# Performance work log

Hardware: AMD Instinct MI355X
Metric: run time of the kernel (lower is better)

The kernel has to match this reference:

```python
import jax, jax.numpy as jnp
import numpy as np

EMB = 1024
H = 16
D = EMB // H  # 64
EPS = 1e-5
SM_SCALE = 1.0  # forward default sm_scale=1.0
CAUSAL = True
NEG = -1e30


def _layernorm(t, g, b):
    # LayerNorm over last dim (head_dim), per torch nn.LayerNorm(head_dim)
    m = jnp.mean(t, axis=-1, keepdims=True)
    v = jnp.mean(jnp.square(t - m), axis=-1, keepdims=True)
    return (t - m) * jax.lax.rsqrt(v + EPS) * g + b


def setup_inputs() -> dict:
    key = jax.random.key(0)
    ks = jax.random.split(key, 8)
    N, L = 2, 2048
    x = jax.random.normal(ks[0], (N, L, EMB), dtype=jnp.float32)
    mask = jnp.ones((N, L), dtype=jnp.int32)  # accepted but unused, as in the torch module
    s = 0.02
    Wq = jax.random.normal(ks[1], (EMB, EMB), dtype=jnp.float32) * s
    Wk = jax.random.normal(ks[2], (EMB, EMB), dtype=jnp.float32) * s
    Wv = jax.random.normal(ks[3], (EMB, EMB), dtype=jnp.float32) * s
    Wo = jax.random.normal(ks[4], (EMB, EMB), dtype=jnp.float32) * s
    bo = jnp.zeros((EMB,), dtype=jnp.float32)
    gq = jnp.ones((D,), dtype=jnp.float32)
    bq = jnp.zeros((D,), dtype=jnp.float32)
    gk = jnp.ones((D,), dtype=jnp.float32)
    bk = jnp.zeros((D,), dtype=jnp.float32)
    return {"x": x, "mask": mask, "Wq": Wq, "Wk": Wk, "Wv": Wv,
            "gq": gq, "bq": bq, "gk": gk, "bk": bk, "Wo": Wo, "bo": bo}


def reference(x, mask, Wq, Wk, Wv, gq, bq, gk, bk, Wo, bo):
    N, L, _ = x.shape
    # QKV projections (torch Linear: x @ W.T), split into heads -> [N, H, L, D]
    q = (x @ Wq.T).reshape(N, L, H, D).transpose(0, 2, 1, 3)
    k = (x @ Wk.T).reshape(N, L, H, D).transpose(0, 2, 1, 3)
    v = (x @ Wv.T).reshape(N, L, H, D).transpose(0, 2, 1, 3)
    # fused_q_norm variant: per-head LayerNorm on Q and K (fused into attention kernel)
    q = _layernorm(q, gq, bq)
    k = _layernorm(k, gk, bk)
    scores = jnp.einsum('nhld,nhmd->nhlm', q, k) * SM_SCALE  # [N,H,L,L]
    if CAUSAL:
        causal = jnp.tril(jnp.ones((L, L), dtype=bool))
        scores = jnp.where(causal, scores, NEG)
    attn = jax.nn.softmax(scores, axis=-1)
    out = jnp.einsum('nhlm,nhmd->nhld', attn, v)
    out = out.transpose(0, 2, 1, 3).reshape(N, L, EMB)
    return out @ Wo.T + bo
```

## Files before the change

kernel.cpp:

```cpp
#include <hip/hip_runtime.h>
#include <stdint.h>

typedef unsigned short u16;
typedef u16   u16x4    __attribute__((ext_vector_type(4)));
typedef u16   u16x8    __attribute__((ext_vector_type(8)));
typedef u16x8 u16x8_ma __attribute__((may_alias));
typedef __bf16 bf16x8  __attribute__((ext_vector_type(8)));
typedef float f32x4    __attribute__((ext_vector_type(4)));
typedef f32x4 f32x4_ma __attribute__((may_alias));

#define EMB    1024
#define NHEAD  16
#define HD     64
#define SEQ    2048
#define NBATCH 2
#define ROWS   (NBATCH*SEQ)
#define SATT   72
#define TSTRIDE 132

__device__ __forceinline__ u16 f2b(float f) {
  uint32_t u; __builtin_memcpy(&u, &f, 4);
  u = u + 0x7fffu + ((u >> 16) & 1u);
  return (u16)(u >> 16);
}
__device__ __forceinline__ u16x8 ld8(const u16* p) { return *(const u16x8_ma*)p; }
__device__ __forceinline__ void  st8(u16* p, u16x8 v) { *(u16x8_ma*)p = v; }
__device__ __forceinline__ bf16x8 asbf(u16x8 v) {
  union { u16x8 u; bf16x8 b; } c; c.u = v; return c.b;
}
__device__ __forceinline__ uint32_t cvtpk(float a, float b) {
  uint32_t r;
  asm("v_cvt_pk_bf16_f32 %0, %1, %2" : "=v"(r) : "v"(a), "v"(b));
  return r;
}
__device__ __forceinline__ void async_cp16(const u16* g, u16* l) {
  __builtin_amdgcn_global_load_lds(
      (const __attribute__((address_space(1))) void*)g,
      (__attribute__((address_space(3))) void*)l, 16, 0, 0);
}

__global__ __launch_bounds__(256) void cvt_all(
    const float* __restrict__ x,
    const float* __restrict__ w0, const float* __restrict__ w1,
    const float* __restrict__ w2, const float* __restrict__ w3,
    u16* __restrict__ xd, u16* __restrict__ d0, u16* __restrict__ d1,
    u16* __restrict__ d2, u16* __restrict__ d3)
{
  int bid = blockIdx.x;
  const float* s; u16* d; int off;
  if (bid < 4096) { s = x; d = xd; off = bid; }
  else {
    int t = bid - 4096; int m = t >> 10; off = t & 1023;
    switch (m) {
      case 0: s = w0; d = d0; break;
      case 1: s = w1; d = d1; break;
      case 2: s = w2; d = d2; break;
      default: s = w3; d = d3; break;
    }
  }
  size_t i = ((size_t)off * 256 + threadIdx.x) * 4;
  f32x4 v = *(const f32x4_ma*)(s + i);
  u16x4 o;
  #pragma unroll
  for (int j = 0; j < 4; j++) o[j] = f2b(v[j]);
  *(u16x4*)(d + i) = o;
}

template<int AMODE>
__device__ __forceinline__ void gemm_acc_128x128(
    const u16* __restrict__ A, const u16* __restrict__ B,
    int m0, int n0, u16* As, u16* Bs, f32x4 acc[4][4])
{
  const int tid  = threadIdx.x;
  const int lane = tid & 63;
  const int wave = tid >> 6;
  const int wm   = (wave >> 1) * 64;
  const int wn   = (wave & 1) * 64;
  const int ar   = tid >> 2;
  const int ac   = (tid & 3) * 8;
  const int lm   = lane & 15;
  const int lk   = (lane >> 4) * 8;

  #pragma unroll
  for (int i = 0; i < 4; i++)
    #pragma unroll
    for (int j = 0; j < 4; j++)
      #pragma unroll
      for (int e = 0; e < 4; e++) acc[i][j][e] = 0.f;

  for (int k0 = 0; k0 < EMB; k0 += 64) {
    size_t a0[2], a1[2];
    #pragma unroll
    for (int pnl = 0; pnl < 2; pnl++) {
      int kc = k0 + pnl * 32 + ac;
      if (AMODE == 0) {
        a0[pnl] = (size_t)(m0 + ar)      * EMB + kc;
        a1[pnl] = (size_t)(m0 + ar + 64) * EMB + kc;
      } else {
        int h = kc >> 6, d = kc & 63;
        int r0 = m0 + ar, r1 = m0 + ar + 64;
        a0[pnl] = (((size_t)((r0 >> 11) * NHEAD + h)) * SEQ + (r0 & (SEQ-1))) * HD + d;
        a1[pnl] = (((size_t)((r1 >> 11) * NHEAD + h)) * SEQ + (r1 & (SEQ-1))) * HD + d;
      }
    }
    __syncthreads();
    #pragma unroll
    for (int pnl = 0; pnl < 2; pnl++) {
      const int pb = pnl * 4096;
      async_cp16(A + a0[pnl], As + pb + tid * 8);
      async_cp16(A + a1[pnl], As + pb + (tid + 256) * 8);
      async_cp16(B + (size_t)(n0 + ar)      * EMB + k0 + pnl * 32 + ac, Bs + pb + tid * 8);
      async_cp16(B + (size_t)(n0 + ar + 64) * EMB + k0 + pnl * 32 + ac, Bs + pb + (tid + 256) * 8);
    }
    __syncthreads();

    #pragma unroll
    for (int pnl = 0; pnl < 2; pnl++) {
      const int pb = pnl * 4096;
      bf16x8 af[4], bfr[4];
      #pragma unroll
      for (int i = 0; i < 4; i++)
        af[i] = asbf(ld8(As + pb + (wm + i * 16 + lm) * 32 + lk));
      #pragma unroll
      for (int j = 0; j < 4; j++)
        bfr[j] = asbf(ld8(Bs + pb + (wn + j * 16 + lm) * 32 + lk));
      #pragma unroll
      for (int i = 0; i < 4; i++)
        #pragma unroll
        for (int j = 0; j < 4; j++)
          acc[i][j] = __builtin_amdgcn_mfma_f32_16x16x32_bf16(af[i], bfr[j], acc[i][j], 0, 0, 0);
    }
  }
}

__device__ __forceinline__ void epilogue_scatter_ln(
    f32x4 acc[4][4], u16* dst, int m0, int n0, int head_base, int Hdst,
    const float* g, const float* b, int do_ln)
{
  const int lane = threadIdx.x & 63, wave = threadIdx.x >> 6;
  const int wm = (wave >> 1) * 64, wn = (wave & 1) * 64;
  const int lm = lane & 15, quad = lane >> 4;

  float gv[4], bv[4];
  #pragma unroll
  for (int j = 0; j < 4; j++) { gv[j] = g[j * 16 + lm]; bv[j] = b[j * 16 + lm]; }

  #pragma unroll
  for (int i = 0; i < 4; i++)
    #pragma unroll
    for (int r = 0; r < 4; r++) {
      float val[4];
      #pragma unroll
      for (int j = 0; j < 4; j++) val[j] = acc[i][j][r];
      if (do_ln) {
        float s = val[0] + val[1] + val[2] + val[3];
        #pragma unroll
        for (int o = 8; o >= 1; o >>= 1) s += __shfl_xor(s, o, 64);
        float mean = s * (1.f / 64.f);
        float ss = 0.f;
        #pragma unroll
        for (int j = 0; j < 4; j++) { val[j] -= mean; ss += val[j] * val[j]; }
        #pragma unroll
        for (int o = 8; o >= 1; o >>= 1) ss += __shfl_xor(ss, o, 64);
        float inv = rsqrtf(ss * (1.f / 64.f) + 1e-5f);
        #pragma unroll
        for (int j = 0; j < 4; j++) val[j] = val[j] * inv * gv[j] + bv[j];
      }
      int row = m0 + wm + i * 16 + quad * 4 + r;
      int bn = row >> 11, l = row & (SEQ - 1);
      #pragma unroll
      for (int j = 0; j < 4; j++) {
        int col = n0 + wn + j * 16 + lm;
        int hl = (col >> 6) - head_base, d = col & 63;
        dst[(((size_t)(bn * Hdst + hl)) * SEQ + l) * HD + d] = f2b(val[j]);
      }
    }
}

__device__ __forceinline__ void epilogue_transpose_v(
    f32x4 acc[4][4], u16* dst, int m0, int n0, int Hdst, u16* Ts)
{
  const int tid = threadIdx.x, lane = tid & 63, wave = tid >> 6;
  const int wm = (wave >> 1) * 64;
  const int lm = lane & 15, quad = lane >> 4;
  const int bn = m0 >> 11, l0 = m0 & (SEQ - 1);

  #pragma unroll
  for (int pass = 0; pass < 2; ++pass) {
    __syncthreads();
    if ((wave & 1) == pass) {
      #pragma unroll
      for (int i = 0; i < 4; i++)
        #pragma unroll
        for (int j = 0; j < 4; j++)
          #pragma unroll
          for (int r = 0; r < 4; r++)
            Ts[(j * 16 + lm) * TSTRIDE + wm + i * 16 + quad * 4 + r] =
                f2b(acc[i][j][r]);
    }
    __syncthreads();
    const int hl = (n0 >> 6) + pass;
    u16* base = dst + ((size_t)(bn * Hdst + hl)) * HD * SEQ + l0;
    #pragma unroll
    for (int it = 0; it < 4; ++it) {
      int e = it * 2048 + tid * 8;
      int d = e >> 7, l = e & 127;
      st8(base + (size_t)d * SEQ + l, ld8(Ts + d * TSTRIDE + l));
    }
  }
}

__global__ __launch_bounds__(256) void gemm_qkv(
    const u16* __restrict__ x,
    const u16* __restrict__ Wq, const u16* __restrict__ Wk, const u16* __restrict__ Wv,
    const float* __restrict__ gq, const float* __restrict__ bq,
    const float* __restrict__ gk, const float* __restrict__ bk,
    u16* __restrict__ qd, u16* __restrict__ kb, u16* __restrict__ vb)
{
  __shared__ __align__(16) u16 As[128 * 64];
  __shared__ __align__(16) u16 Bs[128 * 64];
  __shared__ __align__(16) u16 Ts[64 * TSTRIDE];
  const int m0 = blockIdx.y * 128, n0 = blockIdx.x * 128;
  f32x4 acc[4][4];
  if (blockIdx.z == 0) {
    gemm_acc_128x128<0>(x, Wq, m0, n0, As, Bs, acc);
    epilogue_scatter_ln(acc, qd, m0, n0, 0, NHEAD, gq, bq, 1);
  } else if (blockIdx.z == 1) {
    gemm_acc_128x128<0>(x, Wk, m0, n0, As, Bs, acc);
    epilogue_scatter_ln(acc, kb, m0, n0, 0, NHEAD, gk, bk, 1);
  } else {
    gemm_acc_128x128<0>(x, Wv, m0, n0, As, Bs, acc);
    epilogue_transpose_v(acc, vb, m0, n0, NHEAD, Ts);
  }
}

__global__ __launch_bounds__(256) void gemm_q(
    const u16* __restrict__ x, const u16* __restrict__ Wq,
    const float* __restrict__ gq, const float* __restrict__ bq,
    u16* __restrict__ qd)
{
  __shared__ __align__(16) u16 As[128 * 64];
  __shared__ __align__(16) u16 Bs[128 * 64];
  const int m0 = blockIdx.y * 128, n0 = blockIdx.x * 128;
  f32x4 acc[4][4];
  gemm_acc_128x128<0>(x, Wq, m0, n0, As, Bs, acc);
  epilogue_scatter_ln(acc, qd, m0, n0, 0, NHEAD, gq, bq, 1);
}
__global__ __launch_bounds__(256) void gemm_kv(
    const u16* __restrict__ x,
    const u16* __restrict__ Wk, const u16* __restrict__ Wv,
    const float* __restrict__ gk, const float* __restrict__ bk,
    u16* __restrict__ k, u16* __restrict__ v, int head_lo, int hpp)
{
  __shared__ __align__(16) u16 As[128 * 64];
  __shared__ __align__(16) u16 Bs[128 * 64];
  __shared__ __align__(16) u16 Ts[64 * TSTRIDE];
  const int m0 = blockIdx.y * 128, n0 = blockIdx.x * 128;
  const u16* W = (blockIdx.z == 0 ? Wk : Wv) + (size_t)head_lo * HD * EMB;
  f32x4 acc[4][4];
  gemm_acc_128x128<0>(x, W, m0, n0, As, Bs, acc);
  if (blockIdx.z == 0)
    epilogue_scatter_ln(acc, k, m0, n0, 0, hpp, gk, bk, 1);
  else
    epilogue_transpose_v(acc, v, m0, n0, hpp, Ts);
}

__global__ __launch_bounds__(256, 4) void attn(
    u16* qd, const u16* __restrict__ K, const u16* __restrict__ V,
    int head_lo, int hpp)
{
  __shared__ __align__(16) u16 Ks[2][64 * SATT];
  __shared__ __align__(16) u16 Vt[2][64 * SATT];

  const int hl = blockIdx.y, n = blockIdx.z;
  const int perm = (7 * blockIdx.x + (hl & 7) + 8 * n) & 31;
  const int p = perm ^ (31 * (hl >> 3));
  const int tid = threadIdx.x, lane = tid & 63, wave = tid >> 6;
  const int lm = lane & 15, quad = lane >> 4, lk = quad * 8;
  u16* Qh = qd + ((size_t)(n * NHEAD + head_lo + hl)) * SEQ * HD;
  const u16* Kh = K + ((size_t)(n * hpp + hl)) * SEQ * HD;
  const u16* Vh = V + ((size_t)(n * hpp + hl)) * HD * SEQ;

  const int sr = tid >> 3;
  const int sc = (tid & 7) * 8;
  const int vd = tid >> 2;
  const int vc = (tid & 3) * 16;

  bf16x8 aq[2];
  #pragma unroll
  for (int ks = 0; ks < 2; ++ks)
    aq[ks] = asbf(ld8(Qh + (size_t)(p * 64 + wave * 16 + lm) * HD + ks * 32 + lk));

  u16x8 kr0, kr1, vr0, vr1;
  kr0 = ld8(Kh + (size_t)(sr)      * HD + sc);
  kr1 = ld8(Kh + (size_t)(sr + 32) * HD + sc);
  vr0 = ld8(Vh + (size_t)vd * SEQ + vc);
  vr1 = ld8(Vh + (size_t)vd * SEQ + vc + 8);
  st8(&Ks[0][sr * SATT + sc], kr0);
  st8(&Ks[0][(sr + 32) * SATT + sc], kr1);
  st8(&Vt[0][vd * SATT + vc], vr0);
  st8(&Vt[0][vd * SATT + vc + 8], vr1);
  kr0 = ld8(Kh + (size_t)(64 + sr)      * HD + sc);
  kr1 = ld8(Kh + (size_t)(64 + sr + 32) * HD + sc);
  vr0 = ld8(Vh + (size_t)vd * SEQ + 64 + vc);
  vr1 = ld8(Vh + (size_t)vd * SEQ + 64 + vc + 8);
  __syncthreads();

  f32x4 oacc[4];
  #pragma unroll
  for (int j = 0; j < 4; j++)
    #pragma unroll
    for (int e = 0; e < 4; e++) oacc[j][e] = 0.f;
  float m_i = -1e30f, psum = 0.f;

  const int idx0 = (((quad & 1) * 2) * 16 + lm) * 4;
  const int idx1 = idx0 + 64;
  const int qrow = p * 64 + wave * 16 + lm;

  for (int t = 0; t <= p; ++t) {
    const int cur = t & 1;
    if (t < p) {
      const int nb = 1 - cur;
      st8(&Ks[nb][sr * SATT + sc], kr0);
      st8(&Ks[nb][(sr + 32) * SATT + sc], kr1);
      st8(&Vt[nb][vd * SATT + vc], vr0);
      st8(&Vt[nb][vd * SATT + vc + 8], vr1);
      if (t + 1 < p) {
        const size_t base = (size_t)(t + 2) * 64;
        kr0 = ld8(Kh + (base + sr)      * HD + sc);
        kr1 = ld8(Kh + (base + sr + 32) * HD + sc);
        vr0 = ld8(Vh + (size_t)vd * SEQ + base + vc);
        vr1 = ld8(Vh + (size_t)vd * SEQ + base + vc + 8);
      }
    }

    f32x4 s[4];
    #pragma unroll
    for (int j = 0; j < 4; j++)
      #pragma unroll
      for (int e = 0; e < 4; e++) s[j][e] = 0.f;
    __builtin_amdgcn_s_setprio(1);
    #pragma unroll
    for (int ks = 0; ks < 2; ++ks)
      #pragma unroll
      for (int j = 0; j < 4; j++) {
        bf16x8 ak = asbf(ld8(&Ks[cur][(j * 16 + lm) * SATT + ks * 32 + lk]));
        s[j] = __builtin_amdgcn_mfma_f32_16x16x32_bf16(ak, aq[ks], s[j], 0, 0, 0);
      }
    __builtin_amdgcn_s_setprio(0);

    if (t == p) {
      #pragma unroll
      for (int j = 0; j < 4; j++)
        #pragma unroll
        for (int r = 0; r < 4; r++)
          if (t * 64 + j * 16 + quad * 4 + r > qrow) s[j][r] = -1e30f;
    }

    float mx = fmaxf(fmaxf(s[0][0], s[0][1]), fmaxf(s[0][2], s[0][3]));
    #pragma unroll
    for (int j = 1; j < 4; j++)
      mx = fmaxf(mx, fmaxf(fmaxf(s[j][0], s[j][1]), fmaxf(s[j][2], s[j][3])));
    mx = fmaxf(mx, __shfl_xor(mx, 16, 64));
    mx = fmaxf(mx, __shfl_xor(mx, 32, 64));
    const float mnew = fmaxf(m_i, mx);
    const float alpha = __expf(m_i - mnew);
    m_i = mnew;
    float part = 0.f;
    #pragma unroll
    for (int j = 0; j < 4; j++)
      #pragma unroll
      for (int r = 0; r < 4; r++) {
        float pv = __expf(s[j][r] - mnew);
        s[j][r] = pv;
        part += pv;
      }
    psum = psum * alpha + part;

    float ar_[4];
    #pragma unroll
    for (int r = 0; r < 4; r++)
      ar_[r] = __shfl(alpha, (lane & 48) | (quad * 4 + r), 64);
    #pragma unroll
    for (int j = 0; j < 4; j++)
      #pragma unroll
      for (int r = 0; r < 4; r++) oacc[j][r] *= ar_[r];

    uint32_t u[8];
    #pragma unroll
    for (int j = 0; j < 4; j++) {
      u[2 * j]     = cvtpk(s[j][0], s[j][1]);
      u[2 * j + 1] = cvtpk(s[j][2], s[j][3]);
    }

    __builtin_amdgcn_s_setprio(1);
    #pragma unroll
    for (int ks = 0; ks < 2; ++ks) {
      union { uint32_t w[4]; bf16x8 v; } cv;
      #pragma unroll
      for (int w = 0; w < 4; w++) {
        int lo = __builtin_amdgcn_ds_bpermute(w < 2 ? idx0 : idx1,
                                              (int)u[ks * 4 + (w & 1)]);
        int hi = __builtin_amdgcn_ds_bpermute(w < 2 ? idx0 : idx1,
                                              (int)u[ks * 4 + 2 + (w & 1)]);
        cv.w[w] = (quad < 2) ? (uint32_t)lo : (uint32_t)hi;
      }
      bf16x8 ap = cv.v;
      #pragma unroll
      for (int j = 0; j < 4; j++) {
        bf16x8 bv = asbf(ld8(&Vt[cur][(j * 16 + lm) * SATT + ks * 32 + lk]));
        oacc[j] = __builtin_amdgcn_mfma_f32_16x16x32_bf16(ap, bv, oacc[j], 0, 0, 0);
      }
    }
    __builtin_amdgcn_s_setprio(0);
    __syncthreads();
  }

  float s_ = psum;
  s_ += __shfl_xor(s_, 16, 64);
  s_ += __shfl_xor(s_, 32, 64);
  const float inv = 1.0f / s_;
  float ir_[4];
  #pragma unroll
  for (int r = 0; r < 4; r++)
    ir_[r] = __shfl(inv, (lane & 48) | (quad * 4 + r), 64);
  #pragma unroll
  for (int r = 0; r < 4; r++) {
    const int row = p * 64 + wave * 16 + quad * 4 + r;
    #pragma unroll
    for (int j = 0; j < 4; j++)
      Qh[(size_t)row * HD + j * 16 + lm] = f2b(oacc[j][r] * ir_[r]);
  }
}

__global__ __launch_bounds__(256) void gemm_out(
    const u16* __restrict__ ao, const u16* __restrict__ Wo,
    const float* __restrict__ bo, float* __restrict__ out)
{
  __shared__ __align__(16) u16 As[64 * 64];
  __shared__ __align__(16) u16 Bs[128 * 64];
  const int m0 = blockIdx.y * 64, n0 = blockIdx.x * 128;
  const int tid  = threadIdx.x;
  const int lane = tid & 63;
  const int wave = tid >> 6;
  const int wm   = (wave >> 1) * 32;
  const int wn   = (wave & 1) * 64;
  const int ar   = tid >> 2;
  const int ac   = (tid & 3) * 8;
  const int lm   = lane & 15;
  const int lk   = (lane >> 4) * 8;

  f32x4 acc[2][4];
  #pragma unroll
  for (int i = 0; i < 2; i++)
    #pragma unroll
    for (int j = 0; j < 4; j++)
      #pragma unroll
      for (int e = 0; e < 4; e++) acc[i][j][e] = 0.f;

  for (int k0 = 0; k0 < EMB; k0 += 64) {
    size_t aoff[2];
    #pragma unroll
    for (int pnl = 0; pnl < 2; pnl++) {
      int kc = k0 + pnl * 32 + ac, h = kc >> 6, d = kc & 63;
      int r0 = m0 + ar;
      aoff[pnl] = (((size_t)((r0 >> 11) * NHEAD + h)) * SEQ + (r0 & (SEQ-1))) * HD + d;
    }
    __syncthreads();
    #pragma unroll
    for (int pnl = 0; pnl < 2; pnl++) {
      async_cp16(ao + aoff[pnl], As + pnl * 2048 + tid * 8);
      async_cp16(Wo + (size_t)(n0 + ar)      * EMB + k0 + pnl * 32 + ac, Bs + pnl * 4096 + tid * 8);
      async_cp16(Wo + (size_t)(n0 + ar + 64) * EMB + k0 + pnl * 32 + ac, Bs + pnl * 4096 + (tid + 256) * 8);
    }
    __syncthreads();

    #pragma unroll
    for (int pnl = 0; pnl < 2; pnl++) {
      bf16x8 af[2], bfr[4];
      #pragma unroll
      for (int i = 0; i < 2; i++)
        af[i] = asbf(ld8(As + pnl * 2048 + (wm + i * 16 + lm) * 32 + lk));
      #pragma unroll
      for (int j = 0; j < 4; j++)
        bfr[j] = asbf(ld8(Bs + pnl * 4096 + (wn + j * 16 + lm) * 32 + lk));
      #pragma unroll
      for (int i = 0; i < 2; i++)
        #pragma unroll
        for (int j = 0; j < 4; j++)
          acc[i][j] = __builtin_amdgcn_mfma_f32_16x16x32_bf16(af[i], bfr[j], acc[i][j], 0, 0, 0);
    }
  }

  const int quad = lane >> 4;
  #pragma unroll
  for (int j = 0; j < 4; j++) {
    int col = n0 + wn + j * 16 + lm;
    float bias = bo[col];
    #pragma unroll
    for (int i = 0; i < 2; i++)
      #pragma unroll
      for (int r = 0; r < 4; r++) {
        int row = m0 + wm + i * 16 + quad * 4 + r;
        out[(size_t)row * EMB + col] = acc[i][j][r] + bias;
      }
  }
}

extern "C" void kernel_launch(void* const* d_in, const int* in_sizes, int n_in,
                              void* d_out, int out_size, void* d_ws, size_t ws_size,
                              hipStream_t stream)
{
  const float* xf  = (const float*)d_in[0];
  const float* Wqf = (const float*)d_in[2];
  const float* Wkf = (const float*)d_in[3];
  const float* Wvf = (const float*)d_in[4];
  const float* gq  = (const float*)d_in[5];
  const float* bq  = (const float*)d_in[6];
  const float* gk  = (const float*)d_in[7];
  const float* bk  = (const float*)d_in[8];
  const float* Wof = (const float*)d_in[9];
  const float* bo  = (const float*)d_in[10];

  const size_t MB = 1u << 20;
  u16* xb  = (u16*)d_ws;
  u16* wqb = xb  + (size_t)ROWS * EMB;
  u16* wkb = wqb + (size_t)EMB * EMB;
  u16* wvb = wkb + (size_t)EMB * EMB;
  u16* wob = wvb + (size_t)EMB * EMB;
  u16* kvbase = wob + (size_t)EMB * EMB;

  size_t avail = (ws_size > 16 * MB) ? ws_size - 16 * MB : 2 * MB;
  int hpp = NHEAD;
  while ((size_t)hpp * MB > avail && hpp > 2) hpp >>= 1;
  const size_t kv_elems = (size_t)hpp * NBATCH * SEQ * HD;
  u16* kbuf = kvbase;
  u16* vbuf = kbuf + kv_elems;

  u16* qd = (u16*)d_in[0];
  float* out = (float*)d_out;

  cvt_all<<<dim3(8192), 256, 0, stream>>>(xf, Wqf, Wkf, Wvf, Wof,
                                          xb, wqb, wkb, wvb, wob);
  if (hpp == NHEAD) {
    gemm_qkv<<<dim3(8, 32, 3), 256, 0, stream>>>(xb, wqb, wkb, wvb,
                                                 gq, bq, gk, bk,
                                                 qd, kbuf, vbuf);
    attn<<<dim3(32, NHEAD, NBATCH), 256, 0, stream>>>(qd, kbuf, vbuf, 0, NHEAD);
  } else {
    gemm_q<<<dim3(8, 32), 256, 0, stream>>>(xb, wqb, gq, bq, qd);
    for (int g = 0; g < NHEAD / hpp; ++g) {
      gemm_kv<<<dim3(hpp / 2, 32, 2), 256, 0, stream>>>(xb, wkb, wvb, gk, bk,
                                                        kbuf, vbuf, g * hpp, hpp);
      attn<<<dim3(32, hpp, NBATCH), 256, 0, stream>>>(qd, kbuf, vbuf, g * hpp, hpp);
    }
  }
  gemm_out<<<dim3(8, 64), 256, 0, stream>>>(qd, wob, bo, out);
}
```

Baseline: 226.6 us.

## Split QKV GEMM, alias transpose scratch onto operand LDS, add XCD-aware block swizzle

The fused QKV projection kernel becomes a Q/K kernel and a separate V kernel. The V-transpose scratch now reuses the A/B shared-memory buffers instead of a third LDS array, which lowers per-block LDS use so more blocks can be resident. All GEMM kernels also remap block indices so consecutive blocks on the same XCD share operand tiles, aiming for better L2 reuse. The cost is one extra kernel launch and a swizzle that assumes the grid size is divisible by 8.

Result: faster. 206.0 us (-9.1%).

```diff
diff --git a/kernel.cpp b/kernel.cpp
--- a/kernel.cpp
+++ b/kernel.cpp
@@ -37,6 +37,12 @@
   __builtin_amdgcn_global_load_lds(
       (const __attribute__((address_space(1))) void*)g,
       (__attribute__((address_space(3))) void*)l, 16, 0, 0);
+}
+__device__ __forceinline__ void xcd_swz(int gx, int gy, int &bx, int &by) {
+  int lin = bx + gx * by;
+  int q = (gx * gy) >> 3;
+  int w = (lin & 7) * q + (lin >> 3);
+  bx = w % gx; by = w / gx;
 }
 
 __global__ __launch_bounds__(256) void cvt_all(
@@ -210,28 +216,41 @@
   }
 }
 
-__global__ __launch_bounds__(256) void gemm_qkv(
+__global__ __launch_bounds__(256) void gemm_qk(
     const u16* __restrict__ x,
-    const u16* __restrict__ Wq, const u16* __restrict__ Wk, const u16* __restrict__ Wv,
+    const u16* __restrict__ Wq, const u16* __restrict__ Wk,
     const float* __restrict__ gq, const float* __restrict__ bq,
     const float* __restrict__ gk, const float* __restrict__ bk,
-    u16* __restrict__ qd, u16* __restrict__ kb, u16* __restrict__ vb)
+    u16* __restrict__ qd, u16* __restrict__ kb)
 {
   __shared__ __align__(16) u16 As[128 * 64];
   __shared__ __align__(16) u16 Bs[128 * 64];
-  __shared__ __align__(16) u16 Ts[64 * TSTRIDE];
-  const int m0 = blockIdx.y * 128, n0 = blockIdx.x * 128;
+  int bx = blockIdx.x, by = blockIdx.y;
+  xcd_swz(8, 32, bx, by);
+  const int m0 = by * 128, n0 = bx * 128;
   f32x4 acc[4][4];
   if (blockIdx.z == 0) {
     gemm_acc_128x128<0>(x, Wq, m0, n0, As, Bs, acc);
     epilogue_scatter_ln(acc, qd, m0, n0, 0, NHEAD, gq, bq, 1);
-  } else if (blockIdx.z == 1) {
+  } else {
     gemm_acc_128x128<0>(x, Wk, m0, n0, As, Bs, acc);
     epilogue_scatter_ln(acc, kb, m0, n0, 0, NHEAD, gk, bk, 1);
-  } else {
-    gemm_acc_128x128<0>(x, Wv, m0, n0, As, Bs, acc);
-    epilogue_transpose_v(acc, vb, m0, n0, NHEAD, Ts);
-  }
+  }
+}
+
+__global__ __launch_bounds__(256) void gemm_v(
+    const u16* __restrict__ x, const u16* __restrict__ Wv,
+    u16* __restrict__ vb)
+{
+  __shared__ __align__(16) u16 buf[128 * 64 * 2];
+  u16* As = buf;
+  u16* Bs = buf + 128 * 64;
+  int bx = blockIdx.x, by = blockIdx.y;
+  xcd_swz(8, 32, bx, by);
+  const int m0 = by * 128, n0 = bx * 128;
+  f32x4 acc[4][4];
+  gemm_acc_128x128<0>(x, Wv, m0, n0, As, Bs, acc);
+  epilogue_transpose_v(acc, vb, m0, n0, NHEAD, buf);
 }
 
 __global__ __launch_bounds__(256) void gemm_q(
@@ -241,7 +260,9 @@
 {
   __shared__ __align__(16) u16 As[128 * 64];
   __shared__ __align__(16) u16 Bs[128 * 64];
-  const int m0 = blockIdx.y * 128, n0 = blockIdx.x * 128;
+  int bx = blockIdx.x, by = blockIdx.y;
+  xcd_swz(8, 32, bx, by);
+  const int m0 = by * 128, n0 = bx * 128;
   f32x4 acc[4][4];
   gemm_acc_128x128<0>(x, Wq, m0, n0, As, Bs, acc);
   epilogue_scatter_ln(acc, qd, m0, n0, 0, NHEAD, gq, bq, 1);
@@ -252,17 +273,19 @@
     const float* __restrict__ gk, const float* __restrict__ bk,
     u16* __restrict__ k, u16* __restrict__ v, int head_lo, int hpp)
 {
-  __shared__ __align__(16) u16 As[128 * 64];
-  __shared__ __align__(16) u16 Bs[128 * 64];
-  __shared__ __align__(16) u16 Ts[64 * TSTRIDE];
-  const int m0 = blockIdx.y * 128, n0 = blockIdx.x * 128;
+  __shared__ __align__(16) u16 buf[128 * 64 * 2];
+  u16* As = buf;
+  u16* Bs = buf + 128 * 64;
+  int bx = blockIdx.x, by = blockIdx.y;
+  xcd_swz(hpp / 2, 32, bx, by);
+  const int m0 = by * 128, n0 = bx * 128;
   const u16* W = (blockIdx.z == 0 ? Wk : Wv) + (size_t)head_lo * HD * EMB;
   f32x4 acc[4][4];
   gemm_acc_128x128<0>(x, W, m0, n0, As, Bs, acc);
   if (blockIdx.z == 0)
     epilogue_scatter_ln(acc, k, m0, n0, 0, hpp, gk, bk, 1);
   else
-    epilogue_transpose_v(acc, v, m0, n0, hpp, Ts);
+    epilogue_transpose_v(acc, v, m0, n0, hpp, buf);
 }
 
 __global__ __launch_bounds__(256, 4) void attn(
@@ -439,7 +462,9 @@
 {
   __shared__ __align__(16) u16 As[64 * 64];
   __shared__ __align__(16) u16 Bs[128 * 64];
-  const int m0 = blockIdx.y * 64, n0 = blockIdx.x * 128;
+  int bx = blockIdx.x, by = blockIdx.y;
+  xcd_swz(8, 64, bx, by);
+  const int m0 = by * 64, n0 = bx * 128;
   const int tid  = threadIdx.x;
   const int lane = tid & 63;
   const int wave = tid >> 6;
@@ -543,9 +568,9 @@
   cvt_all<<<dim3(8192), 256, 0, stream>>>(xf, Wqf, Wkf, Wvf, Wof,
                                           xb, wqb, wkb, wvb, wob);
   if (hpp == NHEAD) {
-    gemm_qkv<<<dim3(8, 32, 3), 256, 0, stream>>>(xb, wqb, wkb, wvb,
-                                                 gq, bq, gk, bk,
-                                                 qd, kbuf, vbuf);
+    gemm_qk<<<dim3(8, 32, 2), 256, 0, stream>>>(xb, wqb, wkb,
+                                                gq, bq, gk, bk, qd, kbuf);
+    gemm_v<<<dim3(8, 32), 256, 0, stream>>>(xb, wvb, vbuf);
     attn<<<dim3(32, NHEAD, NBATCH), 256, 0, stream>>>(qd, kbuf, vbuf, 0, NHEAD);
   } else {
     gemm_q<<<dim3(8, 32), 256, 0, stream>>>(xb, wqb, gq, bq, qd);
```
